# Kernel optimization log

Hardware: AMD Instinct MI355X
Metric: run time of the kernel (lower is better)

## Reference

```python
import jax, jax.numpy as jnp
import numpy as np

B_IMG, B_CAP, T_CAP, D = 64, 64, 64, 1024
H = D // 8          # CBN MLP bottleneck (k=8)
T_IMG = 36          # fixed number of image regions; cap_embed truncated to this
EPS = 1e-5          # BatchNorm eps
GAMMA = 10.0        # softmax gate temperature (norm_output=True)


def _l2norm(x, axis=-1):
    return x / jnp.linalg.norm(x, axis=axis, keepdims=True)


def setup_inputs() -> dict:
    key = jax.random.key(0)
    ks = jax.random.split(key, 8)
    s1 = 1.0 / np.sqrt(D)
    s2 = 1.0 / np.sqrt(H)
    return {
        "img_embed": jax.random.normal(ks[0], (B_IMG, T_IMG, D), jnp.float32),
        "cap_embed": jax.random.normal(ks[1], (B_CAP, T_CAP, D), jnp.float32),
        "lens": jax.random.randint(ks[2], (B_CAP,), 1, T_CAP + 1).astype(jnp.int32),
        # CondBatchNorm1d gamma/beta predictor MLPs: Linear(D,H)->ReLU->Linear(H,D)
        "Wg1": jax.random.normal(ks[3], (D, H), jnp.float32) * s1,
        "bg1": jnp.zeros((H,), jnp.float32),
        "Wg2": jax.random.normal(ks[4], (H, D), jnp.float32) * s2,
        "bg2": jnp.zeros((D,), jnp.float32),
        "Wb1": jax.random.normal(ks[5], (D, H), jnp.float32) * s1,
        "bb1": jnp.zeros((H,), jnp.float32),
        "Wb2": jax.random.normal(ks[6], (H, D), jnp.float32) * s2,
        "bb2": jnp.zeros((D,), jnp.float32),
    }


def reference(img_embed, cap_embed, lens, Wg1, bg1, Wg2, bg2, Wb1, bb1, Wb2, bb2):
    # permute to channels-first and truncate captions to 36 timesteps
    cap = jnp.transpose(cap_embed, (0, 2, 1))[:, :, :T_IMG]   # (Bc, D, 36)
    img = jnp.transpose(img_embed, (0, 2, 1))                 # (Bi, D, 36)
    img_repr = img.mean(-1)                                   # (Bi, D)

    # BatchNorm1d (affine=False), training-mode batch stats over (Bc, T) per channel.
    # cap is identical across the original per-image loop, so normalize once.
    mu = cap.mean(axis=(0, 2), keepdims=True)
    var = cap.var(axis=(0, 2), keepdims=True)
    xn = (cap - mu) / jnp.sqrt(var + EPS)                     # (Bc, D, 36)

    # condition-dependent gamma/beta per image (CBN: 1 + delta_gamma)
    gam = 1.0 + (jax.nn.relu(img_repr @ Wg1 + bg1) @ Wg2 + bg2)   # (Bi, D)
    bet = jax.nn.relu(img_repr @ Wb1 + bb1) @ Wb2 + bb2           # (Bi, D)

    # vectorized over the original Python loop: (Bi, Bc, D, 36)
    txt = gam[:, None, :, None] * xn[None] + bet[:, None, :, None]
    mask = jax.nn.softmax(txt * GAMMA, axis=-1)               # gate over time axis
    txt_vec = (mask * txt).mean(-1)                           # (Bi, Bc, D)

    txt_vec = _l2norm(txt_vec, -1)
    img_vec = _l2norm(img_repr, -1)                           # (Bi, D)
    sims = jnp.einsum("id,ibd->ib", img_vec, txt_vec)        # (Bi, Bc)
    return sims
```

## Files before the change

kernel.cpp:

```cpp
#include <hip/hip_runtime.h>
#include <hip/hip_bf16.h>

#define BI 64
#define BC 64
#define TCAP 64
#define D 1024
#define H 128
#define TIMG 36

__global__ __launch_bounds__(256) void k_pre(const float* __restrict__ img,
                                             const float* __restrict__ cap,
                                             const float* __restrict__ Wg1,
                                             const float* __restrict__ Wb1,
                                             float* __restrict__ repr,
                                             float* __restrict__ ivec,
                                             float* __restrict__ part,
                                             float* __restrict__ W1T) {
    int blk = blockIdx.x, tid = threadIdx.x;
    if (blk < 64) {
        int i = blk;
        const float* base = img + (size_t)i * TIMG * D;
        float s[4] = {0.f, 0.f, 0.f, 0.f};
        for (int t = 0; t < TIMG; ++t) {
#pragma unroll
            for (int r = 0; r < 4; ++r) s[r] += base[t * D + r * 256 + tid];
        }
        float local = 0.f;
#pragma unroll
        for (int r = 0; r < 4; ++r) {
            s[r] *= (1.f / 36.f);
            repr[i * D + r * 256 + tid] = s[r];
            local += s[r] * s[r];
        }
        for (int off = 32; off; off >>= 1) local += __shfl_xor(local, off);
        __shared__ float red[4];
        int wave = tid >> 6;
        if ((tid & 63) == 0) red[wave] = local;
        __syncthreads();
        float inv = rsqrtf(red[0] + red[1] + red[2] + red[3]);
#pragma unroll
        for (int r = 0; r < 4; ++r) ivec[i * D + r * 256 + tid] = s[r] * inv;
    } else if (blk < 320) {
        int idx = blk - 64;
        int b = idx >> 2;
        int d = (idx & 3) * 256 + tid;
        const float* base = cap + (size_t)b * TCAP * D;
        float s = 0.f, ss = 0.f;
#pragma unroll 4
        for (int t = 0; t < TIMG; ++t) {
            float x = base[t * D + d];
            s += x;
            ss += x * x;
        }
        part[b * 2048 + d] = s;
        part[b * 2048 + 1024 + d] = ss;
    } else {
        __shared__ float tile[64][65];
        int idx = blk - 320;
        int bx = idx & 15, by = (idx >> 4) & 1, bz = idx >> 5;
        const float* W = bz ? Wb1 : Wg1;
        int d0 = bx * 64, c0 = by * 64;
        int lane = tid & 63, w = tid >> 6;
#pragma unroll
        for (int k = 0; k < 16; ++k) {
            int dl = k * 4 + w;
            tile[dl][lane] = W[(size_t)(d0 + dl) * H + c0 + lane];
        }
        __syncthreads();
#pragma unroll
        for (int k = 0; k < 16; ++k) {
            int cl = k * 4 + w;
            W1T[(size_t)(bz * 128 + c0 + cl) * D + d0 + lane] = tile[lane][cl];
        }
    }
}

__global__ __launch_bounds__(256) void k_mid(const float* __restrict__ part,
                                             const float* __restrict__ repr,
                                             const float* __restrict__ W1T,
                                             const float* __restrict__ bg1,
                                             const float* __restrict__ bb1,
                                             float* __restrict__ mu,
                                             float* __restrict__ istd,
                                             float* __restrict__ hid) {
    int blk = blockIdx.x, tid = threadIdx.x;
    if (blk < 4) {
        int d = blk * 256 + tid;
        float s = 0.f, ss = 0.f;
        for (int g = 0; g < BC; ++g) {
            s += part[g * 2048 + d];
            ss += part[g * 2048 + 1024 + d];
        }
        const float invN = 1.f / 2304.f;
        float m = s * invN;
        float v = ss * invN - m * m;
        mu[d] = m;
        istd[d] = rsqrtf(v + 1e-5f);
    } else {
        int o = (blk - 4) * 4 + (tid >> 6);
        int lane = tid & 63;
        int i = o >> 8, c = o & 255;
        const float* r = repr + (size_t)i * D;
        const float* w = W1T + (size_t)c * D;
        float acc = 0.f;
#pragma unroll
        for (int k = 0; k < 16; ++k) acc = fmaf(r[k * 64 + lane], w[k * 64 + lane], acc);
        for (int off = 32; off; off >>= 1) acc += __shfl_xor(acc, off);
        if (lane == 0) {
            float b = (c < 128) ? bg1[c] : bb1[c - 128];
            hid[o] = fmaxf(acc + b, 0.f);
        }
    }
}

__global__ __launch_bounds__(256) void k_out(const float* __restrict__ hid,
                                             const float* __restrict__ Wg2, const float* __restrict__ bg2,
                                             const float* __restrict__ Wb2, const float* __restrict__ bb2,
                                             float* __restrict__ gam, float* __restrict__ bet) {
    int i = blockIdx.x >> 2;
    int d = (blockIdx.x & 3) * 256 + threadIdx.x;
    __shared__ float h[256];
    h[threadIdx.x] = hid[i * 256 + threadIdx.x];
    __syncthreads();
    float g = bg2[d], bb = bb2[d];
#pragma unroll 4
    for (int hh = 0; hh < H; ++hh) {
        g = fmaf(h[hh], Wg2[(size_t)hh * D + d], g);
        bb = fmaf(h[128 + hh], Wb2[(size_t)hh * D + d], bb);
    }
    gam[(size_t)i * D + d] = 1.f + g;
    bet[(size_t)i * D + d] = bb;
}

__global__ __launch_bounds__(512) void k_main(const float* __restrict__ cap,
                                              const float* __restrict__ mu,
                                              const float* __restrict__ istd,
                                              const float* __restrict__ gam,
                                              const float* __restrict__ bet,
                                              const float* __restrict__ ivec,
                                              float* __restrict__ out) {
    int b = blockIdx.x, ig = blockIdx.y, tid = threadIdx.x;
    int d0 = tid, d1 = tid + 512;
    const float* base = cap + (size_t)b * TCAP * D;
    float m0 = mu[d0], m1 = mu[d1];
    float is0 = istd[d0], is1 = istd[d1];
    float x0[TIMG], x1[TIMG];
#pragma unroll
    for (int t = 0; t < TIMG; ++t) {
        x0[t] = (base[t * D + d0] - m0) * is0;
        x1[t] = (base[t * D + d1] - m1) * is1;
    }
    __shared__ float redS[8][8], redD[8][8];
    const float A = 14.4269504089f;
    const float INV = 0.0693147180560f;
    int wave = tid >> 6;
#pragma unroll
    for (int k = 0; k < 8; ++k) {
        int i = ig * 8 + k;
        float g0 = gam[i * D + d0], g1 = gam[i * D + d1];
        float be0 = bet[i * D + d0], be1 = bet[i * D + d1];
        float a0 = A * g0, a1 = A * g1;
        float c0 = A * (be0 - 6.f), c1 = A * (be1 - 6.f);
        float sw0 = 0.f, sxa0 = 0.f, sw1 = 0.f, sxa1 = 0.f;
#pragma unroll
        for (int t = 0; t < TIMG; ++t) {
            float arg0 = fmaf(a0, x0[t], c0);
            float e0 = __builtin_amdgcn_exp2f(arg0);
            sw0 += e0;
            sxa0 = fmaf(e0, arg0, sxa0);
            float arg1 = fmaf(a1, x1[t], c1);
            float e1 = __builtin_amdgcn_exp2f(arg1);
            sw1 += e1;
            sxa1 = fmaf(e1, arg1, sxa1);
        }
        float tv0 = fmaf(INV, sxa0 / sw0, 6.f);
        float tv1 = fmaf(INV, sxa1 / sw1, 6.f);
        float iv0 = ivec[i * D + d0], iv1 = ivec[i * D + d1];
        float ss = tv0 * tv0 + tv1 * tv1;
        float sd = iv0 * tv0 + iv1 * tv1;
        for (int off = 32; off; off >>= 1) {
            ss += __shfl_xor(ss, off);
            sd += __shfl_xor(sd, off);
        }
        if ((tid & 63) == 0) { redS[k][wave] = ss; redD[k][wave] = sd; }
    }
    __syncthreads();
    if (tid < 64) {
        int k = tid >> 3, w = tid & 7;
        float s = redS[k][w], d = redD[k][w];
#pragma unroll
        for (int off = 1; off < 8; off <<= 1) {
            s += __shfl_xor(s, off);
            d += __shfl_xor(d, off);
        }
        if (w == 0) {
            int i = ig * 8 + k;
            out[i * BC + b] = d * rsqrtf(s);
        }
    }
}

extern "C" void kernel_launch(void* const* d_in, const int* in_sizes, int n_in,
                              void* d_out, int out_size, void* d_ws, size_t ws_size,
                              hipStream_t stream) {
    const float* img = (const float*)d_in[0];
    const float* cap = (const float*)d_in[1];
    const float* Wg1 = (const float*)d_in[3];
    const float* bg1 = (const float*)d_in[4];
    const float* Wg2 = (const float*)d_in[5];
    const float* bg2 = (const float*)d_in[6];
    const float* Wb1 = (const float*)d_in[7];
    const float* bb1 = (const float*)d_in[8];
    const float* Wb2 = (const float*)d_in[9];
    const float* bb2 = (const float*)d_in[10];

    float* ws = (float*)d_ws;
    float* repr = ws;
    float* ivec = ws + 65536;
    float* gam  = ws + 131072;
    float* bet  = ws + 196608;
    float* mu   = ws + 262144;
    float* istd = ws + 263168;
    float* part = ws + 264192;
    float* W1T  = ws + 395264;
    float* hid  = ws + 657408;
    float* out = (float*)d_out;

    k_pre<<<dim3(384), dim3(256), 0, stream>>>(img, cap, Wg1, Wb1, repr, ivec, part, W1T);
    k_mid<<<dim3(4100), dim3(256), 0, stream>>>(part, repr, W1T, bg1, bb1, mu, istd, hid);
    k_out<<<dim3(256), dim3(256), 0, stream>>>(hid, Wg2, bg2, Wb2, bb2, gam, bet);
    k_main<<<dim3(BC, 8), dim3(512), 0, stream>>>(cap, mu, istd, gam, bet, ivec, out);
}
```

Baseline: 58.71 us.

## Vectorize loads across kernels and interchange k_main loops to stream caption data

Uses float4/float2 vector loads and stores in the prologue, stats, hidden-layer and output-projection kernels, halving or quartering their block counts to match. In the main kernel, the per-image loop is moved inside the time loop, so each caption element is loaded and normalized once and applied to 8 images held in register accumulators. This removes the 72-float per-thread register array of caption values. In exchange it keeps 64 accumulator/coefficient registers per thread, and each thread now covers adjacent channels (float2) instead of strided ones.

```diff
diff --git a/kernel.cpp b/kernel.cpp
--- a/kernel.cpp
+++ b/kernel.cpp
@@ -19,44 +19,38 @@
     int blk = blockIdx.x, tid = threadIdx.x;
     if (blk < 64) {
         int i = blk;
-        const float* base = img + (size_t)i * TIMG * D;
-        float s[4] = {0.f, 0.f, 0.f, 0.f};
+        const float4* base = (const float4*)(img + (size_t)i * TIMG * D);
+        float4 s = {0.f, 0.f, 0.f, 0.f};
         for (int t = 0; t < TIMG; ++t) {
-#pragma unroll
-            for (int r = 0; r < 4; ++r) s[r] += base[t * D + r * 256 + tid];
-        }
-        float local = 0.f;
-#pragma unroll
-        for (int r = 0; r < 4; ++r) {
-            s[r] *= (1.f / 36.f);
-            repr[i * D + r * 256 + tid] = s[r];
-            local += s[r] * s[r];
-        }
+            float4 v = base[t * 256 + tid];
+            s.x += v.x; s.y += v.y; s.z += v.z; s.w += v.w;
+        }
+        s.x *= (1.f / 36.f); s.y *= (1.f / 36.f); s.z *= (1.f / 36.f); s.w *= (1.f / 36.f);
+        ((float4*)(repr + (size_t)i * D))[tid] = s;
+        float local = s.x * s.x + s.y * s.y + s.z * s.z + s.w * s.w;
         for (int off = 32; off; off >>= 1) local += __shfl_xor(local, off);
         __shared__ float red[4];
         int wave = tid >> 6;
         if ((tid & 63) == 0) red[wave] = local;
         __syncthreads();
         float inv = rsqrtf(red[0] + red[1] + red[2] + red[3]);
-#pragma unroll
-        for (int r = 0; r < 4; ++r) ivec[i * D + r * 256 + tid] = s[r] * inv;
-    } else if (blk < 320) {
-        int idx = blk - 64;
-        int b = idx >> 2;
-        int d = (idx & 3) * 256 + tid;
-        const float* base = cap + (size_t)b * TCAP * D;
-        float s = 0.f, ss = 0.f;
-#pragma unroll 4
+        float4 o = {s.x * inv, s.y * inv, s.z * inv, s.w * inv};
+        ((float4*)(ivec + (size_t)i * D))[tid] = o;
+    } else if (blk < 128) {
+        int b = blk - 64;
+        const float4* base = (const float4*)(cap + (size_t)b * TCAP * D);
+        float4 s = {0.f, 0.f, 0.f, 0.f}, ss = {0.f, 0.f, 0.f, 0.f};
         for (int t = 0; t < TIMG; ++t) {
-            float x = base[t * D + d];
-            s += x;
-            ss += x * x;
-        }
-        part[b * 2048 + d] = s;
-        part[b * 2048 + 1024 + d] = ss;
+            float4 v = base[t * 256 + tid];
+            s.x += v.x; s.y += v.y; s.z += v.z; s.w += v.w;
+            ss.x = fmaf(v.x, v.x, ss.x); ss.y = fmaf(v.y, v.y, ss.y);
+            ss.z = fmaf(v.z, v.z, ss.z); ss.w = fmaf(v.w, v.w, ss.w);
+        }
+        ((float4*)(part + b * 2048))[tid] = s;
+        ((float4*)(part + b * 2048 + 1024))[tid] = ss;
     } else {
         __shared__ float tile[64][65];
-        int idx = blk - 320;
+        int idx = blk - 128;
         int bx = idx & 15, by = (idx >> 4) & 1, bz = idx >> 5;
         const float* W = bz ? Wb1 : Wg1;
         int d0 = bx * 64, c0 = by * 64;
@@ -100,11 +94,18 @@
         int o = (blk - 4) * 4 + (tid >> 6);
         int lane = tid & 63;
         int i = o >> 8, c = o & 255;
-        const float* r = repr + (size_t)i * D;
-        const float* w = W1T + (size_t)c * D;
+        const float4* r = (const float4*)(repr + (size_t)i * D);
+        const float4* w = (const float4*)(W1T + (size_t)c * D);
         float acc = 0.f;
 #pragma unroll
-        for (int k = 0; k < 16; ++k) acc = fmaf(r[k * 64 + lane], w[k * 64 + lane], acc);
+        for (int k = 0; k < 4; ++k) {
+            float4 rv = r[k * 64 + lane];
+            float4 wv = w[k * 64 + lane];
+            acc = fmaf(rv.x, wv.x, acc);
+            acc = fmaf(rv.y, wv.y, acc);
+            acc = fmaf(rv.z, wv.z, acc);
+            acc = fmaf(rv.w, wv.w, acc);
+        }
         for (int off = 32; off; off >>= 1) acc += __shfl_xor(acc, off);
         if (lane == 0) {
             float b = (c < 128) ? bg1[c] : bb1[c - 128];
@@ -117,19 +118,26 @@
                                              const float* __restrict__ Wg2, const float* __restrict__ bg2,
                                              const float* __restrict__ Wb2, const float* __restrict__ bb2,
                                              float* __restrict__ gam, float* __restrict__ bet) {
-    int i = blockIdx.x >> 2;
-    int d = (blockIdx.x & 3) * 256 + threadIdx.x;
+    int i = blockIdx.x >> 1;
+    int d2 = (blockIdx.x & 1) * 256 + threadIdx.x;
     __shared__ float h[256];
     h[threadIdx.x] = hid[i * 256 + threadIdx.x];
     __syncthreads();
-    float g = bg2[d], bb = bb2[d];
+    float2 g = ((const float2*)bg2)[d2];
+    float2 bb = ((const float2*)bb2)[d2];
 #pragma unroll 4
     for (int hh = 0; hh < H; ++hh) {
-        g = fmaf(h[hh], Wg2[(size_t)hh * D + d], g);
-        bb = fmaf(h[128 + hh], Wb2[(size_t)hh * D + d], bb);
-    }
-    gam[(size_t)i * D + d] = 1.f + g;
-    bet[(size_t)i * D + d] = bb;
+        float2 wg = ((const float2*)(Wg2 + (size_t)hh * D))[d2];
+        float2 wb = ((const float2*)(Wb2 + (size_t)hh * D))[d2];
+        float hg = h[hh], hb = h[128 + hh];
+        g.x = fmaf(hg, wg.x, g.x);
+        g.y = fmaf(hg, wg.y, g.y);
+        bb.x = fmaf(hb, wb.x, bb.x);
+        bb.y = fmaf(hb, wb.y, bb.y);
+    }
+    float2 go = {1.f + g.x, 1.f + g.y};
+    ((float2*)(gam + (size_t)i * D))[d2] = go;
+    ((float2*)(bet + (size_t)i * D))[d2] = bb;
 }
 
 __global__ __launch_bounds__(512) void k_main(const float* __restrict__ cap,
@@ -140,44 +148,52 @@
                                               const float* __restrict__ ivec,
                                               float* __restrict__ out) {
     int b = blockIdx.x, ig = blockIdx.y, tid = threadIdx.x;
-    int d0 = tid, d1 = tid + 512;
-    const float* base = cap + (size_t)b * TCAP * D;
-    float m0 = mu[d0], m1 = mu[d1];
-    float is0 = istd[d0], is1 = istd[d1];
-    float x0[TIMG], x1[TIMG];
-#pragma unroll
-    for (int t = 0; t < TIMG; ++t) {
-        x0[t] = (base[t * D + d0] - m0) * is0;
-        x1[t] = (base[t * D + d1] - m1) * is1;
-    }
-    __shared__ float redS[8][8], redD[8][8];
+    const float2* base = (const float2*)(cap + (size_t)b * TCAP * D);
+    float2 mu2 = ((const float2*)mu)[tid];
+    float2 is2 = ((const float2*)istd)[tid];
     const float A = 14.4269504089f;
     const float INV = 0.0693147180560f;
-    int wave = tid >> 6;
+
+    float a0[8], a1[8], c0[8], c1[8];
+    float sw0[8], sw1[8], sxa0[8], sxa1[8];
 #pragma unroll
     for (int k = 0; k < 8; ++k) {
         int i = ig * 8 + k;
-        float g0 = gam[i * D + d0], g1 = gam[i * D + d1];
-        float be0 = bet[i * D + d0], be1 = bet[i * D + d1];
-        float a0 = A * g0, a1 = A * g1;
-        float c0 = A * (be0 - 6.f), c1 = A * (be1 - 6.f);
-        float sw0 = 0.f, sxa0 = 0.f, sw1 = 0.f, sxa1 = 0.f;
-#pragma unroll
-        for (int t = 0; t < TIMG; ++t) {
-            float arg0 = fmaf(a0, x0[t], c0);
+        float2 g = ((const float2*)(gam + (size_t)i * D))[tid];
+        float2 be = ((const float2*)(bet + (size_t)i * D))[tid];
+        a0[k] = A * g.x;
+        a1[k] = A * g.y;
+        c0[k] = A * (be.x - 6.f);
+        c1[k] = A * (be.y - 6.f);
+        sw0[k] = 0.f; sw1[k] = 0.f; sxa0[k] = 0.f; sxa1[k] = 0.f;
+    }
+#pragma unroll 4
+    for (int t = 0; t < TIMG; ++t) {
+        float2 cp = base[t * 512 + tid];
+        float x0 = (cp.x - mu2.x) * is2.x;
+        float x1 = (cp.y - mu2.y) * is2.y;
+#pragma unroll
+        for (int k = 0; k < 8; ++k) {
+            float arg0 = fmaf(a0[k], x0, c0[k]);
             float e0 = __builtin_amdgcn_exp2f(arg0);
-            sw0 += e0;
-            sxa0 = fmaf(e0, arg0, sxa0);
-            float arg1 = fmaf(a1, x1[t], c1);
+            sw0[k] += e0;
+            sxa0[k] = fmaf(e0, arg0, sxa0[k]);
+            float arg1 = fmaf(a1[k], x1, c1[k]);
             float e1 = __builtin_amdgcn_exp2f(arg1);
-            sw1 += e1;
-            sxa1 = fmaf(e1, arg1, sxa1);
-        }
-        float tv0 = fmaf(INV, sxa0 / sw0, 6.f);
-        float tv1 = fmaf(INV, sxa1 / sw1, 6.f);
-        float iv0 = ivec[i * D + d0], iv1 = ivec[i * D + d1];
+            sw1[k] += e1;
+            sxa1[k] = fmaf(e1, arg1, sxa1[k]);
+        }
+    }
+    __shared__ float redS[8][8], redD[8][8];
+    int wave = tid >> 6;
+#pragma unroll
+    for (int k = 0; k < 8; ++k) {
+        int i = ig * 8 + k;
+        float2 iv = ((const float2*)(ivec + (size_t)i * D))[tid];
+        float tv0 = fmaf(INV, sxa0[k] / sw0[k], 6.f);
+        float tv1 = fmaf(INV, sxa1[k] / sw1[k], 6.f);
         float ss = tv0 * tv0 + tv1 * tv1;
-        float sd = iv0 * tv0 + iv1 * tv1;
+        float sd = iv.x * tv0 + iv.y * tv1;
         for (int off = 32; off; off >>= 1) {
             ss += __shfl_xor(ss, off);
             sd += __shfl_xor(sd, off);
@@ -226,8 +242,8 @@
     float* hid  = ws + 657408;
     float* out = (float*)d_out;
 
-    k_pre<<<dim3(384), dim3(256), 0, stream>>>(img, cap, Wg1, Wb1, repr, ivec, part, W1T);
+    k_pre<<<dim3(192), dim3(256), 0, stream>>>(img, cap, Wg1, Wb1, repr, ivec, part, W1T);
     k_mid<<<dim3(4100), dim3(256), 0, stream>>>(part, repr, W1T, bg1, bb1, mu, istd, hid);
-    k_out<<<dim3(256), dim3(256), 0, stream>>>(hid, Wg2, bg2, Wb2, bb2, gam, bet);
+    k_out<<<dim3(128), dim3(256), 0, stream>>>(hid, Wg2, bg2, Wb2, bb2, gam, bet);
     k_main<<<dim3(BC, 8), dim3(512), 0, stream>>>(cap, mu, istd, gam, bet, ivec, out);
 }
```

New measurement: 55.44 us. 5.6% less time.
